# Optimization experiments

Hardware: AMD Instinct MI355X
Metric: run time of the kernel (lower is better)

## Reference

```python
import jax, jax.numpy as jnp
import numpy as np

NEG_SLOPE = 0.2  # PyG GATConv default leaky_relu slope


def gat_conv(x, src, dst, W, att_s, att_d, bias, concat):
    """Single PyG-style GATConv (eval mode, self-loops already in src/dst).
    x: [N, F_in]; W: [F_in, H*D]; att_s, att_d: [H, D]; bias: [H*D] or [D]."""
    N = x.shape[0]
    H, D = att_s.shape
    h = (x @ W).reshape(N, H, D)                      # [N,H,D]
    a_s = (h * att_s[None]).sum(-1)                   # [N,H]
    a_d = (h * att_d[None]).sum(-1)                   # [N,H]
    e = a_s[src] + a_d[dst]                           # [E,H]
    e = jnp.where(e > 0, e, NEG_SLOPE * e)            # leaky_relu
    # edge softmax over incoming edges of each destination node
    m = jax.ops.segment_max(e, dst, num_segments=N)
    m = jnp.where(jnp.isfinite(m), m, 0.0)
    ex = jnp.exp(e - m[dst])
    denom = jax.ops.segment_sum(ex, dst, num_segments=N)
    alpha = ex / (denom[dst] + 1e-16)                 # [E,H]
    out = jax.ops.segment_sum(alpha[:, :, None] * h[src], dst, num_segments=N)  # [N,H,D]
    out = out.reshape(N, H * D) if concat else out.mean(axis=1)
    return out + bias


def setup_inputs() -> dict:
    key = jax.random.key(0)
    ks = jax.random.split(key, 16)
    B, N, E, F = 4, 4096, 131072, 768
    HID, HEADS, C = 64, 4, 6
    s = 0.05
    inp = {
        'node_feat': jax.random.normal(ks[0], (B, N, F), jnp.float32),
        'labels': jax.random.randint(ks[1], (B,), 0, C, jnp.int32),
        'edge_index': jax.random.randint(ks[2], (B, 2, E), 0, N, jnp.int32),
        'W1': jax.random.normal(ks[3], (F, HEADS * HID), jnp.float32) * s,
        'as1': jax.random.normal(ks[4], (HEADS, HID), jnp.float32) * s,
        'ad1': jax.random.normal(ks[5], (HEADS, HID), jnp.float32) * s,
        'b1': jnp.zeros((HEADS * HID,), jnp.float32),
        'W2': jax.random.normal(ks[6], (HEADS * HID, HEADS * HID), jnp.float32) * s,
        'as2': jax.random.normal(ks[7], (HEADS, HID), jnp.float32) * s,
        'ad2': jax.random.normal(ks[8], (HEADS, HID), jnp.float32) * s,
        'b2': jnp.zeros((HEADS * HID,), jnp.float32),
        # gat3: 256 -> 64, 1 head, mean (concat=False)
        'W3': jax.random.normal(ks[9], (HEADS * HID, HID), jnp.float32) * s,
        'as3': jax.random.normal(ks[10], (1, HID), jnp.float32) * s,
        'ad3': jax.random.normal(ks[11], (1, HID), jnp.float32) * s,
        'b3': jnp.zeros((HID,), jnp.float32),
        # classifier
        'Wc': jax.random.normal(ks[12], (HID, C), jnp.float32) * s,
        'bc': jnp.zeros((C,), jnp.float32),
    }
    return inp


def reference(node_feat, labels, edge_index, W1, as1, ad1, b1, W2, as2, ad2, b2, W3, as3, ad3, b3, Wc, bc):
    B, N, _ = node_feat.shape
    loops = jnp.arange(N, dtype=edge_index.dtype)

    def single_graph(x, ei):
        # PyG GATConv adds self-loops by default
        src = jnp.concatenate([ei[0], loops])
        dst = jnp.concatenate([ei[1], loops])
        h = jax.nn.elu(gat_conv(x, src, dst, W1, as1, ad1, b1, True))
        h = jax.nn.elu(gat_conv(h, src, dst, W2, as2, ad2, b2, True))
        h = gat_conv(h, src, dst, W3, as3, ad3, b3, False)
        graph_embed = h.mean(axis=0)                  # [HID]
        return graph_embed @ Wc + bc                  # [C]

    logits = jax.vmap(single_graph)(node_feat, edge_index)   # [B,C]
    logp = jax.nn.log_softmax(logits, axis=-1)
    loss = -logp[jnp.arange(B), labels].mean()
    pred = jnp.argmax(logits, axis=1)
    return (pred, labels, loss)
```

## Files before the change

kernel.cpp:

```cpp
#include <hip/hip_runtime.h>
#include <math.h>

#define B_ 4
#define N_ 4096
#define E_ 131072
#define ET_ (E_ + N_)
#define H_ 4
#define HD_ 256
#define C_ 6

typedef short  s16x8  __attribute__((ext_vector_type(8)));
typedef __bf16 bf16x8 __attribute__((ext_vector_type(8)));
typedef float  f32x4  __attribute__((ext_vector_type(4)));

__device__ inline unsigned short f2bf(float f){
  unsigned u = __builtin_bit_cast(unsigned, f);
  return (unsigned short)((u + 0x7FFFu + ((u >> 16) & 1u)) >> 16);
}
__device__ inline float bf2f(unsigned short s){
  unsigned u = ((unsigned)s) << 16;
  return __builtin_bit_cast(float, u);
}
__device__ inline void split2(float f, short& hi, short& lo){
  unsigned short h = f2bf(f);
  hi = (short)h;
  lo = (short)f2bf(f - bf2f(h));
}
__device__ inline f32x4 mfma_bf16(s16x8 a, s16x8 b, f32x4 c){
  return __builtin_amdgcn_mfma_f32_16x16x32_bf16(
      __builtin_bit_cast(bf16x8, a), __builtin_bit_cast(bf16x8, b), c, 0, 0, 0);
}

__global__ void k_count(const int* __restrict__ ei, int* __restrict__ counts){
  int idx = blockIdx.x*256 + threadIdx.x;
  if (idx >= B_*ET_) return;
  int b = idx / ET_, i = idx - b*ET_;
  int dst = (i < E_) ? ei[b*2*E_ + E_ + i] : (i - E_);
  atomicAdd(&counts[b*N_ + dst], 1);
}

__global__ void k_scan(const int* __restrict__ counts, int* __restrict__ offs){
  __shared__ int lds[1024];
  int b = blockIdx.x, t = threadIdx.x;
  int c[4]; int tot = 0;
  #pragma unroll
  for (int j=0;j<4;j++){ c[j] = counts[b*N_ + t*4 + j]; tot += c[j]; }
  lds[t] = tot; __syncthreads();
  for (int off=1; off<1024; off<<=1){
    int u = (t>=off) ? lds[t-off] : 0;
    __syncthreads();
    lds[t] += u;
    __syncthreads();
  }
  int excl = lds[t] - tot;
  int o = excl;
  #pragma unroll
  for (int j=0;j<4;j++){ offs[b*(N_+1) + t*4 + j] = o; o += c[j]; }
  if (t==1023) offs[b*(N_+1) + N_] = o;
}

__global__ void k_scatter(const int* __restrict__ ei, const int* __restrict__ offs,
                          int* __restrict__ cursor, unsigned short* __restrict__ srcs){
  int idx = blockIdx.x*256 + threadIdx.x;
  if (idx >= B_*ET_) return;
  int b = idx / ET_, i = idx - b*ET_;
  int src, dst;
  if (i < E_){ src = ei[b*2*E_ + i]; dst = ei[b*2*E_ + E_ + i]; }
  else { src = i - E_; dst = src; }
  int pos = offs[b*(N_+1) + dst] + atomicAdd(&cursor[b*N_ + dst], 1);
  srcs[b*ET_ + pos] = (unsigned short)src;
}

__global__ void k_splitT(const float* __restrict__ w, short* __restrict__ hit,
                         short* __restrict__ lot, int K, int NC){
  int idx = blockIdx.x*256 + threadIdx.x;
  if (idx >= K*NC) return;
  int nn = idx / K, kk = idx - nn*K;
  float f = w[(size_t)kk*NC + nn];
  short h, l; split2(f, h, l);
  hit[idx] = h; lot[idx] = l;
}

template<int K, bool AFP32>
__global__ __launch_bounds__(256) void k_mfma(const float* __restrict__ Af,
    const short* __restrict__ Ah, const short* __restrict__ Al,
    const short* __restrict__ Bh, const short* __restrict__ Bl,
    float* __restrict__ O, int NC){
  __shared__ short tAh[64][32], tAl[64][32], tBh[64][32], tBl[64][32];
  int t = threadIdx.x;
  int m0 = blockIdx.x*64, n0 = blockIdx.y*64;
  int r = t >> 2, c = t & 3;
  int cs = (c ^ ((r >> 1) & 3)) * 8;
  int w = t >> 6, l = t & 63;
  int wr = w >> 1, wc = w & 1, g = l >> 4, li = l & 15;
  int rA = wr*32 + li, rB = wc*32 + li;
  int cA = (g ^ ((rA >> 1) & 3)) * 8;
  int cB = (g ^ ((rB >> 1) & 3)) * 8;
  f32x4 z = {0.f,0.f,0.f,0.f};
  f32x4 acc00=z, acc01=z, acc10=z, acc11=z;

  s16x8 vah, vaL, vbh, vbl;
  auto loadSlice = [&](int k0){
    if constexpr (AFP32){
      const float* ap = &Af[(size_t)(m0+r)*K + k0 + c*8];
      float4 f0 = *reinterpret_cast<const float4*>(ap);
      float4 f1 = *reinterpret_cast<const float4*>(ap+4);
      float fv[8] = {f0.x,f0.y,f0.z,f0.w,f1.x,f1.y,f1.z,f1.w};
      #pragma unroll
      for (int j=0;j<8;j++){ short hh,ll; split2(fv[j],hh,ll); vah[j]=hh; vaL[j]=ll; }
    } else {
      vah = *reinterpret_cast<const s16x8*>(&Ah[(size_t)(m0+r)*K + k0 + c*8]);
      vaL = *reinterpret_cast<const s16x8*>(&Al[(size_t)(m0+r)*K + k0 + c*8]);
    }
    vbh = *reinterpret_cast<const s16x8*>(&Bh[(size_t)(n0+r)*K + k0 + c*8]);
    vbl = *reinterpret_cast<const s16x8*>(&Bl[(size_t)(n0+r)*K + k0 + c*8]);
  };

  loadSlice(0);
  for (int k0 = 0; k0 < K; k0 += 32){
    __syncthreads();
    *reinterpret_cast<s16x8*>(&tAh[r][cs]) = vah;
    *reinterpret_cast<s16x8*>(&tAl[r][cs]) = vaL;
    *reinterpret_cast<s16x8*>(&tBh[r][cs]) = vbh;
    *reinterpret_cast<s16x8*>(&tBl[r][cs]) = vbl;
    __syncthreads();
    if (k0 + 32 < K) loadSlice(k0 + 32);
    s16x8 a0h = *reinterpret_cast<const s16x8*>(&tAh[rA   ][cA]);
    s16x8 a1h = *reinterpret_cast<const s16x8*>(&tAh[rA+16][cA]);
    s16x8 a0l = *reinterpret_cast<const s16x8*>(&tAl[rA   ][cA]);
    s16x8 a1l = *reinterpret_cast<const s16x8*>(&tAl[rA+16][cA]);
    s16x8 b0h = *reinterpret_cast<const s16x8*>(&tBh[rB   ][cB]);
    s16x8 b1h = *reinterpret_cast<const s16x8*>(&tBh[rB+16][cB]);
    s16x8 b0l = *reinterpret_cast<const s16x8*>(&tBl[rB   ][cB]);
    s16x8 b1l = *reinterpret_cast<const s16x8*>(&tBl[rB+16][cB]);
    acc00 = mfma_bf16(a0h, b0h, acc00);
    acc00 = mfma_bf16(a0h, b0l, acc00);
    acc00 = mfma_bf16(a0l, b0h, acc00);
    acc01 = mfma_bf16(a0h, b1h, acc01);
    acc01 = mfma_bf16(a0h, b1l, acc01);
    acc01 = mfma_bf16(a0l, b1h, acc01);
    acc10 = mfma_bf16(a1h, b0h, acc10);
    acc10 = mfma_bf16(a1h, b0l, acc10);
    acc10 = mfma_bf16(a1l, b0h, acc10);
    acc11 = mfma_bf16(a1h, b1h, acc11);
    acc11 = mfma_bf16(a1h, b1l, acc11);
    acc11 = mfma_bf16(a1l, b1h, acc11);
  }
  f32x4 accs[2][2] = {{acc00, acc01},{acc10, acc11}};
  #pragma unroll
  for (int mi=0; mi<2; mi++)
    #pragma unroll
    for (int ni=0; ni<2; ni++){
      int row = m0 + wr*32 + mi*16 + 4*g;
      int col = n0 + wc*32 + ni*16 + li;
      #pragma unroll
      for (int j=0; j<4; j++)
        O[(size_t)(row+j)*NC + col] = accs[mi][ni][j];
    }
}

template<int HD, int H>
__global__ void k_attn(const float* __restrict__ h, const float* __restrict__ atts,
                       const float* __restrict__ attd, float* __restrict__ a_s,
                       float* __restrict__ a_d){
  int n = blockIdx.x; int t = threadIdx.x;
  float v = h[(size_t)n*HD + t];
  float ps = v*atts[t], pd = v*attd[t];
  #pragma unroll
  for (int m=32;m>=1;m>>=1){ ps += __shfl_xor(ps,m,64); pd += __shfl_xor(pd,m,64); }
  if ((t&63)==0){ int head = t>>6; a_s[n*H + head]=ps; a_d[n*H + head]=pd; }
}

template<int HD, int H, bool ELU, bool SPLIT>
__global__ __launch_bounds__(256) void k_aggr(const float* __restrict__ h,
    const float* __restrict__ a_s, const float* __restrict__ a_d,
    const unsigned short* __restrict__ srcs, const int* __restrict__ offs,
    const float* __restrict__ bias, float* __restrict__ outf,
    short* __restrict__ outh, short* __restrict__ outl){
  constexpr int VEC = HD/64;
  __shared__ float accL[4][HD];
  __shared__ float psumL[4][H];
  int ng = blockIdx.x;
  int b = ng >> 12, n = ng & (N_-1);
  int t = threadIdx.x;
  int w = t >> 6, l = t & 63;
  int st = offs[b*(N_+1)+n], en = offs[b*(N_+1)+n+1];
  const unsigned short* sp = &srcs[(size_t)b*ET_];
  const float* hb  = &h[(size_t)b*N_*HD];
  const float* asb = &a_s[(size_t)b*N_*H];
  int head = (H==4) ? (l >> 4) : 0;
  float adv = a_d[(size_t)ng*H + head];
  float acc[VEC];
  #pragma unroll
  for (int j=0;j<VEC;j++) acc[j]=0.f;
  float psum = 0.f;

  int i  = st + w;
  int s0 = (i   < en) ? (int)sp[i]   : 0;
  int s1 = (i+4 < en) ? (int)sp[i+4] : 0;
  float hv[VEC], asv;
  if constexpr (VEC==4){
    float4 hq = *reinterpret_cast<const float4*>(&hb[(size_t)s0*HD + l*4]);
    hv[0]=hq.x; hv[1]=hq.y; hv[2]=hq.z; hv[3]=hq.w;
  } else hv[0] = hb[(size_t)s0*HD + l];
  asv = asb[s0*H + head];

  while (i < en){
    int s2 = (i+8 < en) ? (int)sp[i+8] : 0;
    float hn[VEC], asn;
    if constexpr (VEC==4){
      float4 hq = *reinterpret_cast<const float4*>(&hb[(size_t)s1*HD + l*4]);
      hn[0]=hq.x; hn[1]=hq.y; hn[2]=hq.z; hn[3]=hq.w;
    } else hn[0] = hb[(size_t)s1*HD + l];
    asn = asb[s1*H + head];
    float e = asv + adv;
    e = e > 0.f ? e : 0.2f*e;
    float p = __expf(e);
    #pragma unroll
    for (int j=0;j<VEC;j++) acc[j] = fmaf(p, hv[j], acc[j]);
    psum += p;
    #pragma unroll
    for (int j=0;j<VEC;j++) hv[j] = hn[j];
    asv = asn; s1 = s2; i += 4;
  }

  if constexpr (VEC==4){
    *reinterpret_cast<float4*>(&accL[w][l*4]) = make_float4(acc[0],acc[1],acc[2],acc[3]);
  } else accL[w][l] = acc[0];
  if ((l & 15) == 0 && (H==4 || l==0)) psumL[w][head] = psum;
  __syncthreads();
  if (t < HD){
    float a = accL[0][t]+accL[1][t]+accL[2][t]+accL[3][t];
    int h2 = (H==4) ? (t>>6) : 0;
    float ps = psumL[0][h2]+psumL[1][h2]+psumL[2][h2]+psumL[3][h2];
    float val = a/(ps + 1e-16f) + bias[t];
    if (ELU) val = val > 0.f ? val : expm1f(val);
    size_t idx = (size_t)ng*HD + t;
    if (SPLIT){ short hh, ll; split2(val, hh, ll); outh[idx]=hh; outl[idx]=ll; }
    else outf[idx] = val;
  }
}

__global__ void k_reduce(const float* __restrict__ x3, float* __restrict__ embed){
  __shared__ float red[256];
  int bid = blockIdx.x; int b = bid>>4, chunk = bid & 15;
  int t = threadIdx.x; int col = t & 63, q = t>>6;
  float s = 0.f;
  int r0 = chunk*256 + q*64;
  const float* p = &x3[((size_t)b*N_ + r0)*64 + col];
  for (int j=0;j<64;j++) s += p[(size_t)j*64];
  red[t]=s; __syncthreads();
  if (t<64){
    float v = red[t]+red[t+64]+red[t+128]+red[t+192];
    atomicAdd(&embed[b*64+t], v);
  }
}

__global__ void k_final(const float* __restrict__ embed, const float* __restrict__ Wc,
                        const float* __restrict__ bc, const int* __restrict__ labels,
                        float* __restrict__ out){
  __shared__ float lg[B_][C_];
  __shared__ float lossv[B_];
  int t = threadIdx.x;
  if (t < B_*C_){
    int b = t / C_, c = t - b*C_;
    float s = 0.f;
    for (int k=0;k<64;k++) s += embed[b*64+k]*Wc[k*C_+c];
    lg[b][c] = s*(1.0f/N_) + bc[c];
  }
  __syncthreads();
  if (t < B_){
    int b = t;
    float mx = lg[b][0]; int pred = 0;
    for (int c=1;c<C_;c++) if (lg[b][c] > mx){ mx = lg[b][c]; pred = c; }
    float se = 0.f;
    for (int c=0;c<C_;c++) se += expf(lg[b][c]-mx);
    float lse = mx + logf(se);
    int lab = labels[b];
    lossv[b] = lse - lg[b][lab];
    out[b]      = (float)pred;
    out[B_+b]   = (float)lab;
  }
  __syncthreads();
  if (t==0) out[8] = 0.25f*(lossv[0]+lossv[1]+lossv[2]+lossv[3]);
}

extern "C" void kernel_launch(void* const* d_in, const int* in_sizes, int n_in,
                              void* d_out, int out_size, void* d_ws, size_t ws_size,
                              hipStream_t stream){
  const float* x0     = (const float*)d_in[0];
  const int*   labels = (const int*)d_in[1];
  const int*   ei     = (const int*)d_in[2];
  const float* W1=(const float*)d_in[3],  *as1=(const float*)d_in[4],
             *ad1=(const float*)d_in[5],  *b1 =(const float*)d_in[6];
  const float* W2=(const float*)d_in[7],  *as2=(const float*)d_in[8],
             *ad2=(const float*)d_in[9],  *b2 =(const float*)d_in[10];
  const float* W3=(const float*)d_in[11], *as3=(const float*)d_in[12],
             *ad3=(const float*)d_in[13], *b3 =(const float*)d_in[14];
  const float* Wc=(const float*)d_in[15], *bc =(const float*)d_in[16];
  float* out = (float*)d_out;

  char* ws = (char*)d_ws;
  size_t off = 0;
  auto alloc = [&](size_t bytes)->void*{ void* p = ws + off; off += (bytes + 255) & ~(size_t)255; return p; };
  float* hbuf   = (float*)alloc((size_t)B_*N_*HD_*4);
  float* xcur3  = hbuf + (size_t)B_*N_*64;
  float* a_s    = (float*)alloc((size_t)B_*N_*H_*4);
  float* a_d    = (float*)alloc((size_t)B_*N_*H_*4);
  int*   counts = (int*)alloc((size_t)B_*N_*4);
  int*   offs   = (int*)alloc((size_t)B_*(N_+1)*4);
  int*   cursor = (int*)alloc((size_t)B_*N_*4);
  unsigned short* srcs = (unsigned short*)alloc((size_t)B_*ET_*2);
  float* embed  = (float*)alloc((size_t)B_*64*4);
  short* Ah     = (short*)alloc((size_t)B_*N_*HD_*2);
  short* Al     = (short*)alloc((size_t)B_*N_*HD_*2);
  short* Wht    = (short*)alloc((size_t)768*256*2);
  short* Wlt    = (short*)alloc((size_t)768*256*2);

  hipMemsetAsync(counts, 0, (size_t)B_*N_*4, stream);
  hipMemsetAsync(cursor, 0, (size_t)B_*N_*4, stream);
  hipMemsetAsync(embed,  0, (size_t)B_*64*4, stream);

  int nb = (B_*ET_ + 255)/256;
  k_count  <<<nb, 256, 0, stream>>>(ei, counts);
  k_scan   <<<B_, 1024, 0, stream>>>(counts, offs);
  k_scatter<<<nb, 256, 0, stream>>>(ei, offs, cursor, srcs);

  {
    k_splitT<<<(768*256+255)/256, 256, 0, stream>>>(W1, Wht, Wlt, 768, 256);
    k_mfma<768,true><<<dim3(B_*N_/64, 4), 256, 0, stream>>>(x0, nullptr, nullptr,
                                                            Wht, Wlt, hbuf, 256);
    k_attn<256,4><<<B_*N_, 256, 0, stream>>>(hbuf, as1, ad1, a_s, a_d);
    k_aggr<256,4,true,true><<<B_*N_, 256, 0, stream>>>(hbuf, a_s, a_d, srcs, offs, b1,
                                                       nullptr, Ah, Al);
  }
  {
    k_splitT<<<(256*256+255)/256, 256, 0, stream>>>(W2, Wht, Wlt, 256, 256);
    k_mfma<256,false><<<dim3(B_*N_/64, 4), 256, 0, stream>>>(nullptr, Ah, Al,
                                                             Wht, Wlt, hbuf, 256);
    k_attn<256,4><<<B_*N_, 256, 0, stream>>>(hbuf, as2, ad2, a_s, a_d);
    k_aggr<256,4,true,true><<<B_*N_, 256, 0, stream>>>(hbuf, a_s, a_d, srcs, offs, b2,
                                                       nullptr, Ah, Al);
  }
  {
    k_splitT<<<(256*64+255)/256, 256, 0, stream>>>(W3, Wht, Wlt, 256, 64);
    k_mfma<256,false><<<dim3(B_*N_/64, 1), 256, 0, stream>>>(nullptr, Ah, Al,
                                                             Wht, Wlt, hbuf, 64);
    k_attn<64,1><<<B_*N_, 64, 0, stream>>>(hbuf, as3, ad3, a_s, a_d);
    k_aggr<64,1,false,false><<<B_*N_, 256, 0, stream>>>(hbuf, a_s, a_d, srcs, offs, b3,
                                                        xcur3, nullptr, nullptr);
  }

  k_reduce<<<B_*16, 256, 0, stream>>>(xcur3, embed);
  k_final <<<1, 64, 0, stream>>>(embed, Wc, bc, labels, out);
}
```

Before: 396.2 us.

## Fuse attention logits into GEMM epilogue and store projected features as bf16

Folds the per-node attention dot products (a_s, a_d) into the MFMA GEMM epilogue, using 16-lane shuffle reductions plus atomicAdd into pre-zeroed per-layer buffers, and drops the separate k_attn kernels. The projected features h are now stored as bf16 rather than fp32, which halves the gather traffic in the edge-aggregation kernel, the dominant memory cost. This trades accuracy, since messages use bf16-rounded features, and adds atomics plus larger memsets to zero the new buffers.

```diff
diff --git a/kernel.cpp b/kernel.cpp
--- a/kernel.cpp
+++ b/kernel.cpp
@@ -21,6 +21,8 @@
   unsigned u = ((unsigned)s) << 16;
   return __builtin_bit_cast(float, u);
 }
+__device__ inline float bflo(unsigned u){ return __builtin_bit_cast(float, u << 16); }
+__device__ inline float bfhi(unsigned u){ return __builtin_bit_cast(float, u & 0xFFFF0000u); }
 __device__ inline void split2(float f, short& hi, short& lo){
   unsigned short h = f2bf(f);
   hi = (short)h;
@@ -81,14 +83,17 @@
   hit[idx] = h; lot[idx] = l;
 }
 
-template<int K, bool AFP32>
+template<int K, bool AFP32, int H>
 __global__ __launch_bounds__(256) void k_mfma(const float* __restrict__ Af,
     const short* __restrict__ Ah, const short* __restrict__ Al,
     const short* __restrict__ Bh, const short* __restrict__ Bl,
-    float* __restrict__ O, int NC){
+    unsigned short* __restrict__ Ob, int NC,
+    const float* __restrict__ atts, const float* __restrict__ attd,
+    float* __restrict__ a_s, float* __restrict__ a_d){
   __shared__ short tAh[64][32], tAl[64][32], tBh[64][32], tBl[64][32];
   int t = threadIdx.x;
   int m0 = blockIdx.x*64, n0 = blockIdx.y*64;
+  int head = blockIdx.y;
   int r = t >> 2, c = t & 3;
   int cs = (c ^ ((r >> 1) & 3)) * 8;
   int w = t >> 6, l = t & 63;
@@ -147,32 +152,37 @@
     acc11 = mfma_bf16(a1l, b1h, acc11);
   }
   f32x4 accs[2][2] = {{acc00, acc01},{acc10, acc11}};
-  #pragma unroll
-  for (int mi=0; mi<2; mi++)
+  float attsv[2], attdv[2];
+  #pragma unroll
+  for (int ni=0; ni<2; ni++){
+    int colg = n0 + wc*32 + ni*16 + li;
+    attsv[ni] = atts[colg];
+    attdv[ni] = attd[colg];
+  }
+  #pragma unroll
+  for (int mi=0; mi<2; mi++){
     #pragma unroll
-    for (int ni=0; ni<2; ni++){
-      int row = m0 + wr*32 + mi*16 + 4*g;
-      int col = n0 + wc*32 + ni*16 + li;
+    for (int j=0; j<4; j++){
+      int row = m0 + wr*32 + mi*16 + 4*g + j;
+      float sa = accs[mi][0][j]*attsv[0] + accs[mi][1][j]*attsv[1];
+      float sd = accs[mi][0][j]*attdv[0] + accs[mi][1][j]*attdv[1];
       #pragma unroll
-      for (int j=0; j<4; j++)
-        O[(size_t)(row+j)*NC + col] = accs[mi][ni][j];
+      for (int m=1; m<16; m<<=1){ sa += __shfl_xor(sa,m,64); sd += __shfl_xor(sd,m,64); }
+      if (li == 0){
+        atomicAdd(&a_s[(size_t)row*H + head], sa);
+        atomicAdd(&a_d[(size_t)row*H + head], sd);
+      }
+      #pragma unroll
+      for (int ni=0; ni<2; ni++){
+        int col = n0 + wc*32 + ni*16 + li;
+        Ob[(size_t)row*NC + col] = f2bf(accs[mi][ni][j]);
+      }
     }
-}
-
-template<int HD, int H>
-__global__ void k_attn(const float* __restrict__ h, const float* __restrict__ atts,
-                       const float* __restrict__ attd, float* __restrict__ a_s,
-                       float* __restrict__ a_d){
-  int n = blockIdx.x; int t = threadIdx.x;
-  float v = h[(size_t)n*HD + t];
-  float ps = v*atts[t], pd = v*attd[t];
-  #pragma unroll
-  for (int m=32;m>=1;m>>=1){ ps += __shfl_xor(ps,m,64); pd += __shfl_xor(pd,m,64); }
-  if ((t&63)==0){ int head = t>>6; a_s[n*H + head]=ps; a_d[n*H + head]=pd; }
+  }
 }
 
 template<int HD, int H, bool ELU, bool SPLIT>
-__global__ __launch_bounds__(256) void k_aggr(const float* __restrict__ h,
+__global__ __launch_bounds__(256) void k_aggr(const unsigned short* __restrict__ h,
     const float* __restrict__ a_s, const float* __restrict__ a_d,
     const unsigned short* __restrict__ srcs, const int* __restrict__ offs,
     const float* __restrict__ bias, float* __restrict__ outf,
@@ -186,7 +196,7 @@
   int w = t >> 6, l = t & 63;
   int st = offs[b*(N_+1)+n], en = offs[b*(N_+1)+n+1];
   const unsigned short* sp = &srcs[(size_t)b*ET_];
-  const float* hb  = &h[(size_t)b*N_*HD];
+  const unsigned short* hb = &h[(size_t)b*N_*HD];
   const float* asb = &a_s[(size_t)b*N_*H];
   int head = (H==4) ? (l >> 4) : 0;
   float adv = a_d[(size_t)ng*H + head];
@@ -200,18 +210,18 @@
   int s1 = (i+4 < en) ? (int)sp[i+4] : 0;
   float hv[VEC], asv;
   if constexpr (VEC==4){
-    float4 hq = *reinterpret_cast<const float4*>(&hb[(size_t)s0*HD + l*4]);
-    hv[0]=hq.x; hv[1]=hq.y; hv[2]=hq.z; hv[3]=hq.w;
-  } else hv[0] = hb[(size_t)s0*HD + l];
+    uint2 q = *reinterpret_cast<const uint2*>(&hb[(size_t)s0*HD + l*4]);
+    hv[0]=bflo(q.x); hv[1]=bfhi(q.x); hv[2]=bflo(q.y); hv[3]=bfhi(q.y);
+  } else hv[0] = bflo((unsigned)hb[(size_t)s0*HD + l]);
   asv = asb[s0*H + head];
 
   while (i < en){
     int s2 = (i+8 < en) ? (int)sp[i+8] : 0;
     float hn[VEC], asn;
     if constexpr (VEC==4){
-      float4 hq = *reinterpret_cast<const float4*>(&hb[(size_t)s1*HD + l*4]);
-      hn[0]=hq.x; hn[1]=hq.y; hn[2]=hq.z; hn[3]=hq.w;
-    } else hn[0] = hb[(size_t)s1*HD + l];
+      uint2 q = *reinterpret_cast<const uint2*>(&hb[(size_t)s1*HD + l*4]);
+      hn[0]=bflo(q.x); hn[1]=bfhi(q.x); hn[2]=bflo(q.y); hn[3]=bfhi(q.y);
+    } else hn[0] = bflo((unsigned)hb[(size_t)s1*HD + l]);
     asn = asb[s1*H + head];
     float e = asv + adv;
     e = e > 0.f ? e : 0.2f*e;
@@ -303,23 +313,27 @@
   char* ws = (char*)d_ws;
   size_t off = 0;
   auto alloc = [&](size_t bytes)->void*{ void* p = ws + off; off += (bytes + 255) & ~(size_t)255; return p; };
-  float* hbuf   = (float*)alloc((size_t)B_*N_*HD_*4);
-  float* xcur3  = hbuf + (size_t)B_*N_*64;
-  float* a_s    = (float*)alloc((size_t)B_*N_*H_*4);
-  float* a_d    = (float*)alloc((size_t)B_*N_*H_*4);
+  unsigned short* hbuf = (unsigned short*)alloc((size_t)B_*N_*HD_*2);
+  float* xcur3  = (float*)alloc((size_t)B_*N_*64*4);
   int*   counts = (int*)alloc((size_t)B_*N_*4);
+  int*   cursor = (int*)alloc((size_t)B_*N_*4);
   int*   offs   = (int*)alloc((size_t)B_*(N_+1)*4);
-  int*   cursor = (int*)alloc((size_t)B_*N_*4);
   unsigned short* srcs = (unsigned short*)alloc((size_t)B_*ET_*2);
   float* embed  = (float*)alloc((size_t)B_*64*4);
+  float* a_s1   = (float*)alloc((size_t)B_*N_*H_*4);
+  float* a_d1   = (float*)alloc((size_t)B_*N_*H_*4);
+  float* a_s2   = (float*)alloc((size_t)B_*N_*H_*4);
+  float* a_d2   = (float*)alloc((size_t)B_*N_*H_*4);
+  float* a_s3   = (float*)alloc((size_t)B_*N_*4);
+  float* a_d3   = (float*)alloc((size_t)B_*N_*4);
+  size_t zend   = off;
   short* Ah     = (short*)alloc((size_t)B_*N_*HD_*2);
   short* Al     = (short*)alloc((size_t)B_*N_*HD_*2);
   short* Wht    = (short*)alloc((size_t)768*256*2);
   short* Wlt    = (short*)alloc((size_t)768*256*2);
 
-  hipMemsetAsync(counts, 0, (size_t)B_*N_*4, stream);
-  hipMemsetAsync(cursor, 0, (size_t)B_*N_*4, stream);
-  hipMemsetAsync(embed,  0, (size_t)B_*64*4, stream);
+  hipMemsetAsync(counts, 0, (size_t)B_*N_*4*2, stream);
+  hipMemsetAsync(embed,  0, zend - ((char*)embed - ws), stream);
 
   int nb = (B_*ET_ + 255)/256;
   k_count  <<<nb, 256, 0, stream>>>(ei, counts);
@@ -328,26 +342,23 @@
 
   {
     k_splitT<<<(768*256+255)/256, 256, 0, stream>>>(W1, Wht, Wlt, 768, 256);
-    k_mfma<768,true><<<dim3(B_*N_/64, 4), 256, 0, stream>>>(x0, nullptr, nullptr,
-                                                            Wht, Wlt, hbuf, 256);
-    k_attn<256,4><<<B_*N_, 256, 0, stream>>>(hbuf, as1, ad1, a_s, a_d);
-    k_aggr<256,4,true,true><<<B_*N_, 256, 0, stream>>>(hbuf, a_s, a_d, srcs, offs, b1,
+    k_mfma<768,true,4><<<dim3(B_*N_/64, 4), 256, 0, stream>>>(x0, nullptr, nullptr,
+        Wht, Wlt, hbuf, 256, as1, ad1, a_s1, a_d1);
+    k_aggr<256,4,true,true><<<B_*N_, 256, 0, stream>>>(hbuf, a_s1, a_d1, srcs, offs, b1,
                                                        nullptr, Ah, Al);
   }
   {
     k_splitT<<<(256*256+255)/256, 256, 0, stream>>>(W2, Wht, Wlt, 256, 256);
-    k_mfma<256,false><<<dim3(B_*N_/64, 4), 256, 0, stream>>>(nullptr, Ah, Al,
-                                                             Wht, Wlt, hbuf, 256);
-    k_attn<256,4><<<B_*N_, 256, 0, stream>>>(hbuf, as2, ad2, a_s, a_d);
-    k_aggr<256,4,true,true><<<B_*N_, 256, 0, stream>>>(hbuf, a_s, a_d, srcs, offs, b2,
+    k_mfma<256,false,4><<<dim3(B_*N_/64, 4), 256, 0, stream>>>(nullptr, Ah, Al,
+        Wht, Wlt, hbuf, 256, as2, ad2, a_s2, a_d2);
+    k_aggr<256,4,true,true><<<B_*N_, 256, 0, stream>>>(hbuf, a_s2, a_d2, srcs, offs, b2,
                                                        nullptr, Ah, Al);
   }
   {
     k_splitT<<<(256*64+255)/256, 256, 0, stream>>>(W3, Wht, Wlt, 256, 64);
-    k_mfma<256,false><<<dim3(B_*N_/64, 1), 256, 0, stream>>>(nullptr, Ah, Al,
-                                                             Wht, Wlt, hbuf, 64);
-    k_attn<64,1><<<B_*N_, 64, 0, stream>>>(hbuf, as3, ad3, a_s, a_d);
-    k_aggr<64,1,false,false><<<B_*N_, 256, 0, stream>>>(hbuf, a_s, a_d, srcs, offs, b3,
+    k_mfma<256,false,1><<<dim3(B_*N_/64, 1), 256, 0, stream>>>(nullptr, Ah, Al,
+        Wht, Wlt, hbuf, 64, as3, ad3, a_s3, a_d3);
+    k_aggr<64,1,false,false><<<B_*N_, 256, 0, stream>>>(hbuf, a_s3, a_d3, srcs, offs, b3,
                                                         xcur3, nullptr, nullptr);
   }
 
```

New measurement: 376.7 us. 4.9% less time.
